# Kernel tuning notes

Measured on AMD Instinct MI355X. Metric: run time of the kernel, lower is better.

The kernel has to match this reference:

```python
import jax, jax.numpy as jnp
import numpy as np

NUM_HEADS = 8
HEAD_DIM = 64
AVG_K_LENGTH = 20
SCALE = 1.0 / (HEAD_DIM ** 0.5 * float(np.log(AVG_K_LENGTH)))  # 1/(sqrt(dim)*log(avg_k_length))


def setup_inputs() -> dict:
    key = jax.random.key(0)
    k1, k2, k3, k4 = jax.random.split(key, 4)
    B, HD, LQ, LK = 4, NUM_HEADS * HEAD_DIM, 2048, 2048
    q = jax.random.normal(k1, (B, HD, LQ), dtype=jnp.float32)
    k = jax.random.normal(k2, (B, HD, LK), dtype=jnp.float32)
    v = jax.random.normal(k3, (B, HD, LK), dtype=jnp.float32)
    k_length = jax.random.randint(k4, (B,), 512, LK + 1, dtype=jnp.int32)
    return {"q": q, "k": k, "v": v, "k_length": k_length}


def reference(q, k, v, k_length):
    b, hd, lq = q.shape
    lk = k.shape[-1]
    d = hd // NUM_HEADS
    # b (h d) l -> b h d l
    qh = q.reshape(b, NUM_HEADS, d, lq)
    kh = k.reshape(b, NUM_HEADS, d, lk)
    vh = v.reshape(b, NUM_HEADS, d, lk)
    # per-batch entropy-invariance scale: scale * log(k_length)
    s = SCALE * jnp.log(k_length.astype(jnp.float32))[:, None, None, None]  # (b,1,1,1)
    attn = jnp.einsum('bhdq,bhdk->bhqk', qh, kh)  # (b,h,lq,lk)
    attn = jax.nn.softmax(s * attn, axis=-1)
    out = jnp.einsum('bhqk,bhdk->bhdq', attn, vh)  # (b,h,d,lq)
    return out.reshape(b, hd, lq)
```

## Files before the change

### kernel.cpp

```cpp
#include <hip/hip_runtime.h>
#include <hip/hip_bf16.h>
#include <math.h>


typedef __attribute__((ext_vector_type(8))) short short8_t;
typedef __attribute__((ext_vector_type(4))) short short4_t;
typedef __attribute__((ext_vector_type(4))) float float4_t;

#define SEQ   2048
#define NBH   32
#define TQ    64
#define TK    64
#define NKT   (SEQ / TK)

__device__ __forceinline__ unsigned f2bf2u(float a, float b) {
#if __has_builtin(__builtin_amdgcn_cvt_pk_bf16_f32)
  typedef __bf16 bf16x2_t __attribute__((ext_vector_type(2)));
  union { bf16x2_t v; unsigned u; } cv;
  cv.v = __builtin_amdgcn_cvt_pk_bf16_f32(a, b);
  return cv.u;
#else
  union { float f; unsigned u; } x, y;
  x.f = a; y.f = b;
  unsigned ra = x.u + 0x7fffu + ((x.u >> 16) & 1u);
  unsigned rb = y.u + 0x7fffu + ((y.u >> 16) & 1u);
  return (ra >> 16) | (rb & 0xffff0000u);
#endif
}

__device__ __forceinline__ short f2bf1(float a) {
  return (short)(f2bf2u(a, a) & 0xffffu);
}

__device__ __forceinline__ float fast_exp2(float x) {
#if __has_builtin(__builtin_amdgcn_exp2f)
  return __builtin_amdgcn_exp2f(x);
#else
  return exp2f(x);
#endif
}

__device__ __forceinline__ void gld16(const void* g, void* l) {
  __builtin_amdgcn_global_load_lds(
      (const __attribute__((address_space(1))) void*)g,
      (__attribute__((address_space(3))) void*)l, 16, 0, 0);
}

__device__ __forceinline__ float4_t mfma16(short4_t a, short4_t b, float4_t c) {
#if __has_builtin(__builtin_amdgcn_mfma_f32_16x16x16bf16_1k)
  return __builtin_amdgcn_mfma_f32_16x16x16bf16_1k(a, b, c, 0, 0, 0);
#else
  asm("v_mfma_f32_16x16x16_bf16 %0, %1, %2, %0" : "+v"(c) : "v"(a), "v"(b));
  return c;
#endif
}

#define TSTR 68
__global__ __launch_bounds__(256, 8)
void eia_tcast_kernel(const float* __restrict__ in, unsigned short* __restrict__ out,
                      const int* __restrict__ klen, const int do_scale) {
  __shared__ __align__(16) short T[64 * TSTR];
  const int bh = blockIdx.x;
  const int b  = bh >> 3;
  const int l0 = blockIdx.y * 64;
  const int t  = threadIdx.x;
  const int lq = t & 63;
  const int dg = t >> 6;
  float c = 1.0f;
  if (do_scale)
    c = (1.4426950408889634f / (8.0f * 2.9957322735539909f)) * logf((float)klen[b]);
  const size_t ibase = ((size_t)bh * 64) * SEQ + (size_t)(l0 + lq);
#pragma unroll
  for (int dd = 0; dd < 16; dd += 4) {
    const int d = dg * 16 + dd;
    const float f0 = c * in[ibase + (size_t)(d + 0) * SEQ];
    const float f1 = c * in[ibase + (size_t)(d + 1) * SEQ];
    const float f2 = c * in[ibase + (size_t)(d + 2) * SEQ];
    const float f3 = c * in[ibase + (size_t)(d + 3) * SEQ];
    union { short4_t s; unsigned u[2]; } p;
    p.u[0] = f2bf2u(f0, f1);
    p.u[1] = f2bf2u(f2, f3);
    *(short4_t*)&T[lq * TSTR + d] = p.s;
  }
  __syncthreads();
#pragma unroll
  for (int rep = 0; rep < 2; ++rep) {
    const int id = rep * 256 + t;
    const int lr = id >> 3, ch = id & 7;
    union { short8_t v; short4_t h[2]; } o;
    o.h[0] = *(const short4_t*)&T[lr * TSTR + ch * 8];
    o.h[1] = *(const short4_t*)&T[lr * TSTR + ch * 8 + 4];
    *(short8_t*)&out[((size_t)bh * SEQ + l0 + lr) * 64 + ch * 8] = o.v;
  }
}

__global__ __launch_bounds__(256, 8)
void eia_vcast_kernel(const float* __restrict__ in, unsigned short* __restrict__ out) {
  const int i = blockIdx.x * 256 + threadIdx.x;
#pragma unroll
  for (int rep = 0; rep < 2; ++rep) {
    const size_t j = (size_t)(i + rep * 524288) * 4;
    const float4_t f = *(const float4_t*)&in[j];
    union { short4_t s; unsigned u[2]; } p;
    p.u[0] = f2bf2u(f[0], f[1]);
    p.u[1] = f2bf2u(f[2], f[3]);
    *(short4_t*)&out[j] = p.s;
  }
}

__global__ __launch_bounds__(256, 4)
void eia_attn_kernel(const unsigned short* __restrict__ Qt,
                     const unsigned short* __restrict__ Kt,
                     const unsigned short* __restrict__ Vb,
                     float* __restrict__ outg) {
  __shared__ __align__(16) short Ks[2 * TK * 64];
  __shared__ __align__(16) short Vs[2 * 64 * 64];

  const int tid  = threadIdx.x;
  const int bh   = blockIdx.x & 31;
  const int qt   = blockIdx.x >> 5;
  const int q0   = qt * TQ;
  const int w    = tid >> 6;
  const int lane = tid & 63;
  const int quad = lane >> 4;
  const int l16  = lane & 15;
  const int e3   = l16 & 7;
  const int qh   = quad >> 1;
  const int ql   = quad & 1;

  const int lr0 = w * 16 + (lane >> 3);
  const int lr1 = lr0 + 8;
  const int ch0 = (lane & 7) ^ (lr0 & 7);
  const char* kgp0 = (const char*)Kt + (size_t)bh * SEQ * 128 + (size_t)lr0 * 128 + ch0 * 16;
  const char* kgp1 = kgp0 + 8 * 128;
  const char* vgp0 = (const char*)Vb + (size_t)bh * 64 * (SEQ * 2) + (size_t)lr0 * (SEQ * 2) + ch0 * 16;
  const char* vgp1 = vgp0 + 8 * (SEQ * 2);
  short* const kdst0 = &Ks[(w * 16) * 64];
  short* const kdst1 = &Ks[(w * 16 + 8) * 64];
  short* const vdst0 = &Vs[(w * 16) * 64];
  short* const vdst1 = &Vs[(w * 16 + 8) * 64];

  const unsigned short* qrow = Qt + ((size_t)bh * SEQ + q0 + w * 16 + l16) * 64;
  short8_t qfrag[2];
#pragma unroll
  for (int s = 0; s < 2; ++s)
    qfrag[s] = *(const short8_t*)&qrow[s * 32 + quad * 8];

  int kaddr[4][2];
#pragma unroll
  for (int t = 0; t < 4; ++t)
#pragma unroll
    for (int s = 0; s < 2; ++s)
      kaddr[t][s] = (t * 16 + l16) * 64 + ((s * 4 + quad) ^ e3) * 8;
  int vcoff[4];
#pragma unroll
  for (int t = 0; t < 4; ++t)
    vcoff[t] = ((2 * t + qh) ^ e3) * 8 + ql * 4;

  float4_t oacc[4];
#pragma unroll
  for (int t = 0; t < 4; ++t) { oacc[t][0] = 0.f; oacc[t][1] = 0.f; oacc[t][2] = 0.f; oacc[t][3] = 0.f; }
  float lsum = 0.f;

  gld16(kgp0, kdst0); gld16(kgp1, kdst1);
  gld16(vgp0, vdst0); gld16(vgp1, vdst1);
  kgp0 += TK * 128; kgp1 += TK * 128; vgp0 += TK * 2; vgp1 += TK * 2;

  for (int kt = 0; kt < NKT; ++kt) {
    __syncthreads();

    if (kt < NKT - 1) {
      const int nb = ((kt + 1) & 1) * 4096;
      gld16(kgp0, kdst0 + nb); gld16(kgp1, kdst1 + nb);
      gld16(vgp0, vdst0 + nb); gld16(vgp1, vdst1 + nb);
      kgp0 += TK * 128; kgp1 += TK * 128; vgp0 += TK * 2; vgp1 += TK * 2;
    }
    const int cb = (kt & 1) * 4096;

    float4_t sacc[4];
#pragma unroll
    for (int t = 0; t < 4; ++t) { sacc[t][0] = 0.f; sacc[t][1] = 0.f; sacc[t][2] = 0.f; sacc[t][3] = 0.f; }
#pragma unroll
    for (int s = 0; s < 2; ++s)
#pragma unroll
      for (int t = 0; t < 4; ++t) {
        const short8_t kf = *(const short8_t*)&Ks[cb + kaddr[t][s]];
        sacc[t] = __builtin_amdgcn_mfma_f32_16x16x32_bf16(kf, qfrag[s], sacc[t], 0, 0, 0);
      }

    short4_t pb[4];
#pragma unroll
    for (int t = 0; t < 4; ++t) {
      const float e0 = fast_exp2(sacc[t][0]);
      const float e1 = fast_exp2(sacc[t][1]);
      const float e2 = fast_exp2(sacc[t][2]);
      const float e3f = fast_exp2(sacc[t][3]);
      lsum += (e0 + e1) + (e2 + e3f);
      union { short4_t s; unsigned u[2]; } p;
      p.u[0] = f2bf2u(e0, e1);
      p.u[1] = f2bf2u(e2, e3f);
      pb[t] = p.s;
    }

#pragma unroll
    for (int tt = 0; tt < 4; ++tt) {
      const short* vrow = &Vs[cb + (tt * 16 + l16) * 64];
#pragma unroll
      for (int t = 0; t < 4; ++t) {
        const short4_t vf = *(const short4_t*)&vrow[vcoff[t]];
        oacc[tt] = mfma16(vf, pb[t], oacc[tt]);
      }
    }
  }

  float lt = lsum;
  lt += __shfl_xor(lt, 16);
  lt += __shfl_xor(lt, 32);
  const float inv = 1.0f / lt;
  const size_t obase = (size_t)bh * 64 * SEQ + (size_t)(q0 + w * 16 + l16);
#pragma unroll
  for (int tt = 0; tt < 4; ++tt)
#pragma unroll
    for (int r = 0; r < 4; ++r)
      outg[obase + (size_t)(tt * 16 + quad * 4 + r) * SEQ] = oacc[tt][r] * inv;
}

#define DPAD  72
#define PPAD  68
__global__ __launch_bounds__(256, 5)
void eia_attn_fb(const float* __restrict__ qg, const float* __restrict__ kg,
                 const float* __restrict__ vg, const int* __restrict__ klen,
                 float* __restrict__ outg) {
  __shared__ __align__(16) short QPs[TQ * DPAD];
  __shared__ __align__(16) short Ksf[TK * DPAD];
  __shared__ __align__(16) short Vsf[64 * DPAD];

  const int tid  = threadIdx.x;
  const int bh   = blockIdx.x & 31;
  const int qt   = blockIdx.x >> 5;
  const int q0   = qt * TQ;
  const int w    = tid >> 6;
  const int lane = tid & 63;
  const int quad = lane >> 4;
  const int l16  = lane & 15;

  const size_t base = (size_t)bh * 64 * SEQ;
  const float c = (1.4426950408889634f / (8.0f * 2.9957322735539909f)) *
                  logf((float)klen[bh >> 3]);

#pragma unroll
  for (int it = 0; it < 2; ++it) {
    const int e = it * 4 + w;
    float f[8];
#pragma unroll
    for (int j = 0; j < 8; ++j)
      f[j] = c * qg[base + (size_t)(e * 8 + j) * SEQ + (size_t)(q0 + lane)];
    union { short8_t s8; unsigned u[4]; } t;
#pragma unroll
    for (int j = 0; j < 4; ++j) t.u[j] = f2bf2u(f[2 * j], f[2 * j + 1]);
    *(short8_t*)&QPs[lane * DPAD + e * 8] = t.s8;
  }
  __syncthreads();

  short8_t qfrag[2];
#pragma unroll
  for (int s = 0; s < 2; ++s)
    qfrag[s] = *(const short8_t*)&QPs[(w * 16 + l16) * DPAD + s * 32 + quad * 8];

  float4_t oacc[4];
#pragma unroll
  for (int t = 0; t < 4; ++t) { oacc[t][0] = 0.f; oacc[t][1] = 0.f; oacc[t][2] = 0.f; oacc[t][3] = 0.f; }
  float lsumv[4] = {0.f, 0.f, 0.f, 0.f};
  const int pbase = w * (16 * DPAD);

  for (int kt = 0; kt < NKT; ++kt) {
    const int k0 = kt * TK;
#pragma unroll
    for (int it = 0; it < 2; ++it) {
      float f[8];
#pragma unroll
      for (int j = 0; j < 8; ++j)
        f[j] = kg[base + (size_t)((it * 4 + w) * 8 + j) * SEQ + (size_t)(k0 + lane)];
      union { short8_t s8; unsigned u[4]; } t;
#pragma unroll
      for (int j = 0; j < 4; ++j) t.u[j] = f2bf2u(f[2 * j], f[2 * j + 1]);
      *(short8_t*)&Ksf[lane * DPAD + (it * 4 + w) * 8] = t.s8;
    }
#pragma unroll
    for (int it = 0; it < 4; ++it) {
      const int d = it * 16 + (w << 2) + (lane >> 4);
      const float4_t vv = *(const float4_t*)&vg[base + (size_t)d * SEQ + (size_t)(k0 + ((lane & 15) << 2))];
      union { short4_t s4; unsigned u[2]; } t;
      t.u[0] = f2bf2u(vv[0], vv[1]);
      t.u[1] = f2bf2u(vv[2], vv[3]);
      *(short4_t*)&Vsf[d * DPAD + ((lane & 15) << 2)] = t.s4;
    }
    __syncthreads();

    float4_t sacc[4];
#pragma unroll
    for (int t = 0; t < 4; ++t) { sacc[t][0] = 0.f; sacc[t][1] = 0.f; sacc[t][2] = 0.f; sacc[t][3] = 0.f; }
#pragma unroll
    for (int t = 0; t < 4; ++t)
#pragma unroll
      for (int s = 0; s < 2; ++s) {
        const short8_t bf = *(const short8_t*)&Ksf[(t * 16 + l16) * DPAD + s * 32 + quad * 8];
        sacc[t] = __builtin_amdgcn_mfma_f32_16x16x32_bf16(qfrag[s], bf, sacc[t], 0, 0, 0);
      }

#pragma unroll
    for (int r = 0; r < 4; ++r) {
      const float p0 = fast_exp2(sacc[0][r]);
      const float p1 = fast_exp2(sacc[1][r]);
      const float p2 = fast_exp2(sacc[2][r]);
      const float p3 = fast_exp2(sacc[3][r]);
      lsumv[r] += (p0 + p1) + (p2 + p3);
      const int prow = pbase + (quad * 4 + r) * PPAD + l16;
      QPs[prow +  0] = f2bf1(p0);
      QPs[prow + 16] = f2bf1(p1);
      QPs[prow + 32] = f2bf1(p2);
      QPs[prow + 48] = f2bf1(p3);
    }

#pragma unroll
    for (int s = 0; s < 2; ++s) {
      const short* pr = &QPs[pbase + l16 * PPAD + s * 32 + quad * 8];
      const short4_t plo = *(const short4_t*)pr;
      const short4_t phi = *(const short4_t*)(pr + 4);
      const short8_t pf = {plo[0], plo[1], plo[2], plo[3], phi[0], phi[1], phi[2], phi[3]};
#pragma unroll
      for (int t = 0; t < 4; ++t) {
        const short8_t vf = *(const short8_t*)&Vsf[(t * 16 + l16) * DPAD + s * 32 + quad * 8];
        oacc[t] = __builtin_amdgcn_mfma_f32_16x16x32_bf16(pf, vf, oacc[t], 0, 0, 0);
      }
    }
    __syncthreads();
  }

  float inv[4];
#pragma unroll
  for (int r = 0; r < 4; ++r) {
    float v = lsumv[r];
    v += __shfl_xor(v, 1);
    v += __shfl_xor(v, 2);
    v += __shfl_xor(v, 4);
    v += __shfl_xor(v, 8);
    inv[r] = 1.0f / v;
  }
#pragma unroll
  for (int t = 0; t < 4; ++t)
#pragma unroll
    for (int r = 0; r < 4; ++r)
      outg[base + (size_t)(t * 16 + l16) * SEQ +
           (size_t)(q0 + w * 16 + quad * 4 + r)] = oacc[t][r] * inv[r];
}

extern "C" void kernel_launch(void* const* d_in, const int* in_sizes, int n_in,
                              void* d_out, int out_size, void* d_ws, size_t ws_size,
                              hipStream_t stream) {
  const float* q  = (const float*)d_in[0];
  const float* k  = (const float*)d_in[1];
  const float* v  = (const float*)d_in[2];
  const int*   kl = (const int*)d_in[3];
  float* out = (float*)d_out;

  const size_t TEN = (size_t)NBH * SEQ * 64;
  const size_t need = 3 * TEN * sizeof(unsigned short);

  if (ws_size >= need) {
    unsigned short* Qt = (unsigned short*)d_ws;
    unsigned short* Kt = Qt + TEN;
    unsigned short* Vb = Kt + TEN;
    eia_tcast_kernel<<<dim3(32, 32), 256, 0, stream>>>(q, Qt, kl, 1);
    eia_tcast_kernel<<<dim3(32, 32), 256, 0, stream>>>(k, Kt, kl, 0);
    eia_vcast_kernel<<<2048, 256, 0, stream>>>(v, Vb);
    eia_attn_kernel<<<1024, 256, 0, stream>>>(Qt, Kt, Vb, out);
  } else {
    eia_attn_fb<<<1024, 256, 0, stream>>>(q, k, v, kl, out);
  }
}
```

Before: 151.3 us.

## Fuse Q cast into attention, merge K/V prep, double Q tile per block

Merges the K and V bf16 conversion into one prep kernel that writes pre-tiled, fragment-ordered layouts. The Q scale-and-cast now happens inside the attention kernel, which removes the Qt workspace and one launch. The Q tile per block grows to 128 rows, so each wave handles two 16-row groups and reuses every loaded K/V fragment twice. The row sums are now computed with an MFMA against a ones vector instead of VALU adds. In exchange, occupancy drops (launch bounds 2, 512 blocks) and register pressure rises.

```diff
diff --git a/kernel.cpp b/kernel.cpp
--- a/kernel.cpp
+++ b/kernel.cpp
@@ -9,7 +9,7 @@
 
 #define SEQ   2048
 #define NBH   32
-#define TQ    64
+#define TQ    128
 #define TK    64
 #define NKT   (SEQ / TK)
 
@@ -46,6 +46,10 @@
       (__attribute__((address_space(3))) void*)l, 16, 0, 0);
 }
 
+__device__ __forceinline__ float4_t mfma32(short8_t a, short8_t b, float4_t c) {
+  return __builtin_amdgcn_mfma_f32_16x16x32_bf16(a, b, c, 0, 0, 0);
+}
+
 __device__ __forceinline__ float4_t mfma16(short4_t a, short4_t b, float4_t c) {
 #if __has_builtin(__builtin_amdgcn_mfma_f32_16x16x16bf16_1k)
   return __builtin_amdgcn_mfma_f32_16x16x16bf16_1k(a, b, c, 0, 0, 0);
@@ -55,66 +59,76 @@
 #endif
 }
 
-#define TSTR 68
+#define PST 68
 __global__ __launch_bounds__(256, 8)
-void eia_tcast_kernel(const float* __restrict__ in, unsigned short* __restrict__ out,
-                      const int* __restrict__ klen, const int do_scale) {
-  __shared__ __align__(16) short T[64 * TSTR];
-  const int bh = blockIdx.x;
-  const int b  = bh >> 3;
-  const int l0 = blockIdx.y * 64;
-  const int t  = threadIdx.x;
-  const int lq = t & 63;
-  const int dg = t >> 6;
-  float c = 1.0f;
-  if (do_scale)
-    c = (1.4426950408889634f / (8.0f * 2.9957322735539909f)) * logf((float)klen[b]);
-  const size_t ibase = ((size_t)bh * 64) * SEQ + (size_t)(l0 + lq);
-#pragma unroll
-  for (int dd = 0; dd < 16; dd += 4) {
-    const int d = dg * 16 + dd;
-    const float f0 = c * in[ibase + (size_t)(d + 0) * SEQ];
-    const float f1 = c * in[ibase + (size_t)(d + 1) * SEQ];
-    const float f2 = c * in[ibase + (size_t)(d + 2) * SEQ];
-    const float f3 = c * in[ibase + (size_t)(d + 3) * SEQ];
-    union { short4_t s; unsigned u[2]; } p;
-    p.u[0] = f2bf2u(f0, f1);
-    p.u[1] = f2bf2u(f2, f3);
-    *(short4_t*)&T[lq * TSTR + d] = p.s;
-  }
-  __syncthreads();
-#pragma unroll
-  for (int rep = 0; rep < 2; ++rep) {
-    const int id = rep * 256 + t;
-    const int lr = id >> 3, ch = id & 7;
-    union { short8_t v; short4_t h[2]; } o;
-    o.h[0] = *(const short4_t*)&T[lr * TSTR + ch * 8];
-    o.h[1] = *(const short4_t*)&T[lr * TSTR + ch * 8 + 4];
-    *(short8_t*)&out[((size_t)bh * SEQ + l0 + lr) * 64 + ch * 8] = o.v;
-  }
-}
-
-__global__ __launch_bounds__(256, 8)
-void eia_vcast_kernel(const float* __restrict__ in, unsigned short* __restrict__ out) {
-  const int i = blockIdx.x * 256 + threadIdx.x;
-#pragma unroll
-  for (int rep = 0; rep < 2; ++rep) {
-    const size_t j = (size_t)(i + rep * 524288) * 4;
-    const float4_t f = *(const float4_t*)&in[j];
-    union { short4_t s; unsigned u[2]; } p;
-    p.u[0] = f2bf2u(f[0], f[1]);
-    p.u[1] = f2bf2u(f[2], f[3]);
-    *(short4_t*)&out[j] = p.s;
-  }
-}
-
-__global__ __launch_bounds__(256, 4)
-void eia_attn_kernel(const unsigned short* __restrict__ Qt,
-                     const unsigned short* __restrict__ Kt,
-                     const unsigned short* __restrict__ Vb,
+void eia_prep_kernel(const float* __restrict__ kg, const float* __restrict__ vg,
+                     unsigned short* __restrict__ Kt2, unsigned short* __restrict__ Vt2) {
+  __shared__ __align__(16) short T[64 * PST];
+  const int id  = blockIdx.x;
+  const int isV = id >> 10;
+  const int sub = id & 1023;
+  const int bh  = sub >> 5;
+  const int kt  = sub & 31;
+  const int t   = threadIdx.x;
+
+  if (!isV) {
+    const size_t ib = ((size_t)bh * 64) * SEQ + (size_t)(kt * 64) + (t & 63);
+    const int dg = t >> 6;
+#pragma unroll
+    for (int dd = 0; dd < 16; dd += 4) {
+      const int d = dg * 16 + dd;
+      const float f0 = kg[ib + (size_t)(d + 0) * SEQ];
+      const float f1 = kg[ib + (size_t)(d + 1) * SEQ];
+      const float f2 = kg[ib + (size_t)(d + 2) * SEQ];
+      const float f3 = kg[ib + (size_t)(d + 3) * SEQ];
+      union { short4_t s; unsigned u[2]; } p;
+      p.u[0] = f2bf2u(f0, f1);
+      p.u[1] = f2bf2u(f2, f3);
+      *(short4_t*)&T[(t & 63) * PST + d] = p.s;
+    }
+    __syncthreads();
+    unsigned short* outt = Kt2 + (size_t)(bh * 32 + kt) * 4096;
+#pragma unroll
+    for (int rep = 0; rep < 2; ++rep) {
+      const int id2 = rep * 256 + t;
+      const int lr = id2 & 63, ch = id2 >> 6;
+      union { short8_t v; short4_t h[2]; } o;
+      o.h[0] = *(const short4_t*)&T[lr * PST + ch * 8];
+      o.h[1] = *(const short4_t*)&T[lr * PST + ch * 8 + 4];
+      *(short8_t*)&outt[ch * 512 + lr * 8] = o.v;
+    }
+  } else {
+#pragma unroll
+    for (int rep = 0; rep < 4; ++rep) {
+      const int id2 = rep * 256 + t;
+      const int d = id2 >> 4, l4 = (id2 & 15) * 4;
+      const float4_t f = *(const float4_t*)&vg[((size_t)bh * 64 + d) * SEQ + kt * 64 + l4];
+      union { short4_t s; unsigned u[2]; } p;
+      p.u[0] = f2bf2u(f[0], f[1]);
+      p.u[1] = f2bf2u(f[2], f[3]);
+      *(short4_t*)&T[d * PST + l4] = p.s;
+    }
+    __syncthreads();
+    unsigned short* outt = Vt2 + (size_t)(bh * 32 + kt) * 4096;
+#pragma unroll
+    for (int rep = 0; rep < 2; ++rep) {
+      const int c = rep * 256 + t;
+      const int k4 = c >> 5, dp = c & 31;
+      union { short8_t v; short4_t h[2]; } o;
+      o.h[0] = *(const short4_t*)&T[(2 * dp) * PST + k4 * 4];
+      o.h[1] = *(const short4_t*)&T[(2 * dp + 1) * PST + k4 * 4];
+      *(short8_t*)&outt[k4 * 256 + dp * 8] = o.v;
+    }
+  }
+}
+
+__global__ __launch_bounds__(256, 2)
+void eia_attn_kernel(const float* __restrict__ qg,
+                     const unsigned short* __restrict__ Kt2,
+                     const unsigned short* __restrict__ Vt2,
+                     const int* __restrict__ klen,
                      float* __restrict__ outg) {
-  __shared__ __align__(16) short Ks[2 * TK * 64];
-  __shared__ __align__(16) short Vs[2 * 64 * 64];
+  __shared__ __align__(16) short SM[16384];
 
   const int tid  = threadIdx.x;
   const int bh   = blockIdx.x & 31;
@@ -124,105 +138,134 @@
   const int lane = tid & 63;
   const int quad = lane >> 4;
   const int l16  = lane & 15;
-  const int e3   = l16 & 7;
-  const int qh   = quad >> 1;
-  const int ql   = quad & 1;
-
-  const int lr0 = w * 16 + (lane >> 3);
-  const int lr1 = lr0 + 8;
-  const int ch0 = (lane & 7) ^ (lr0 & 7);
-  const char* kgp0 = (const char*)Kt + (size_t)bh * SEQ * 128 + (size_t)lr0 * 128 + ch0 * 16;
-  const char* kgp1 = kgp0 + 8 * 128;
-  const char* vgp0 = (const char*)Vb + (size_t)bh * 64 * (SEQ * 2) + (size_t)lr0 * (SEQ * 2) + ch0 * 16;
-  const char* vgp1 = vgp0 + 8 * (SEQ * 2);
-  short* const kdst0 = &Ks[(w * 16) * 64];
-  short* const kdst1 = &Ks[(w * 16 + 8) * 64];
-  short* const vdst0 = &Vs[(w * 16) * 64];
-  short* const vdst1 = &Vs[(w * 16 + 8) * 64];
-
-  const unsigned short* qrow = Qt + ((size_t)bh * SEQ + q0 + w * 16 + l16) * 64;
-  short8_t qfrag[2];
-#pragma unroll
-  for (int s = 0; s < 2; ++s)
-    qfrag[s] = *(const short8_t*)&qrow[s * 32 + quad * 8];
-
-  int kaddr[4][2];
-#pragma unroll
-  for (int t = 0; t < 4; ++t)
-#pragma unroll
-    for (int s = 0; s < 2; ++s)
-      kaddr[t][s] = (t * 16 + l16) * 64 + ((s * 4 + quad) ^ e3) * 8;
-  int vcoff[4];
-#pragma unroll
-  for (int t = 0; t < 4; ++t)
-    vcoff[t] = ((2 * t + qh) ^ e3) * 8 + ql * 4;
-
-  float4_t oacc[4];
-#pragma unroll
-  for (int t = 0; t < 4; ++t) { oacc[t][0] = 0.f; oacc[t][1] = 0.f; oacc[t][2] = 0.f; oacc[t][3] = 0.f; }
-  float lsum = 0.f;
-
-  gld16(kgp0, kdst0); gld16(kgp1, kdst1);
-  gld16(vgp0, vdst0); gld16(vgp1, vdst1);
-  kgp0 += TK * 128; kgp1 += TK * 128; vgp0 += TK * 2; vgp1 += TK * 2;
-
+
+  const float c = (1.4426950408889634f / (8.0f * 2.9957322735539909f)) *
+                  logf((float)klen[bh >> 3]);
+  const size_t qb = (size_t)bh * 64 * SEQ;
+
+#pragma unroll
+  for (int rep = 0; rep < 8; ++rep) {
+    const int id = rep * 256 + tid;
+    const int d  = id >> 5;
+    const int q4 = (id & 31) * 4;
+    const float4_t f = *(const float4_t*)&qg[qb + (size_t)d * SEQ + (size_t)(q0 + q4)];
+    SM[(q4 + 0) * 68 + d] = f2bf1(c * f[0]);
+    SM[(q4 + 1) * 68 + d] = f2bf1(c * f[1]);
+    SM[(q4 + 2) * 68 + d] = f2bf1(c * f[2]);
+    SM[(q4 + 3) * 68 + d] = f2bf1(c * f[3]);
+  }
+  __syncthreads();
+
+  short8_t qfrag[2][2];
+#pragma unroll
+  for (int g = 0; g < 2; ++g)
+#pragma unroll
+    for (int s = 0; s < 2; ++s) {
+      const short* qp = &SM[(w * 32 + g * 16 + l16) * 68 + s * 32 + quad * 8];
+      const short4_t lo = *(const short4_t*)qp;
+      const short4_t hi = *(const short4_t*)(qp + 4);
+      qfrag[g][s] = short8_t{lo[0], lo[1], lo[2], lo[3], hi[0], hi[1], hi[2], hi[3]};
+    }
+  __syncthreads();
+
+  const char* ktile = (const char*)Kt2 + (size_t)bh * 32 * 8192;
+  const char* vtile = (const char*)Vt2 + (size_t)bh * 32 * 8192;
+  const int i0 = 2 * w, i1 = 2 * w + 1;
+  const char* ks0 = ktile + i0 * 1024 + lane * 16;
+  const char* ks1 = ktile + i1 * 1024 + lane * 16;
+  const char* vs0 = vtile + i0 * 1024 + lane * 16;
+  const char* vs1 = vtile + i1 * 1024 + lane * 16;
+  short* const kd0 = &SM[i0 * 512];
+  short* const kd1 = &SM[i1 * 512];
+  short* const vd0 = &SM[8192 + i0 * 512];
+  short* const vd1 = &SM[8192 + i1 * 512];
+
+  const short* const kf0 = &SM[(0 * 4 + quad) * 512 + l16 * 8];
+  const short* const kf1 = &SM[(1 * 4 + quad) * 512 + l16 * 8];
+  const short* vfp[4];
+#pragma unroll
+  for (int t = 0; t < 4; ++t) vfp[t] = &SM[8192 + (t * 4 + quad) * 256 + l16 * 4];
+
+  const float4_t z4 = {0.f, 0.f, 0.f, 0.f};
+  float4_t oacc[2][4];
+#pragma unroll
+  for (int g = 0; g < 2; ++g)
+#pragma unroll
+    for (int t = 0; t < 4; ++t) oacc[g][t] = z4;
+  float4_t lacc[2] = {z4, z4};
+  const short one_bf = (short)0x3F80;
+  const short4_t ones4 = (l16 == 0) ? short4_t{one_bf, one_bf, one_bf, one_bf}
+                                    : short4_t{0, 0, 0, 0};
+
+  gld16(ks0, kd0); gld16(ks1, kd1);
+  gld16(vs0, vd0); gld16(vs1, vd1);
+  size_t goff = 8192;
+
+#pragma unroll 2
   for (int kt = 0; kt < NKT; ++kt) {
     __syncthreads();
 
     if (kt < NKT - 1) {
-      const int nb = ((kt + 1) & 1) * 4096;
-      gld16(kgp0, kdst0 + nb); gld16(kgp1, kdst1 + nb);
-      gld16(vgp0, vdst0 + nb); gld16(vgp1, vdst1 + nb);
-      kgp0 += TK * 128; kgp1 += TK * 128; vgp0 += TK * 2; vgp1 += TK * 2;
-    }
-    const int cb = (kt & 1) * 4096;
-
-    float4_t sacc[4];
-#pragma unroll
-    for (int t = 0; t < 4; ++t) { sacc[t][0] = 0.f; sacc[t][1] = 0.f; sacc[t][2] = 0.f; sacc[t][3] = 0.f; }
-#pragma unroll
-    for (int s = 0; s < 2; ++s)
+      const int pn = ((kt + 1) & 1) * 4096;
+      gld16(ks0 + goff, kd0 + pn); gld16(ks1 + goff, kd1 + pn);
+      gld16(vs0 + goff, vd0 + pn); gld16(vs1 + goff, vd1 + pn);
+      goff += 8192;
+    }
+    const int par = (kt & 1) * 4096;
+
+    float4_t sac[2][4];
+#pragma unroll
+    for (int t = 0; t < 4; ++t) {
+      const short8_t kv = *(const short8_t*)(kf0 + par + t * 128);
+      sac[0][t] = mfma32(kv, qfrag[0][0], z4);
+      sac[1][t] = mfma32(kv, qfrag[1][0], z4);
+    }
+#pragma unroll
+    for (int t = 0; t < 4; ++t) {
+      const short8_t kv = *(const short8_t*)(kf1 + par + t * 128);
+      sac[0][t] = mfma32(kv, qfrag[0][1], sac[0][t]);
+      sac[1][t] = mfma32(kv, qfrag[1][1], sac[1][t]);
+    }
+
+    short4_t pbf[2][4];
+#pragma unroll
+    for (int g = 0; g < 2; ++g)
 #pragma unroll
       for (int t = 0; t < 4; ++t) {
-        const short8_t kf = *(const short8_t*)&Ks[cb + kaddr[t][s]];
-        sacc[t] = __builtin_amdgcn_mfma_f32_16x16x32_bf16(kf, qfrag[s], sacc[t], 0, 0, 0);
+        const float e0 = fast_exp2(sac[g][t][0]);
+        const float e1 = fast_exp2(sac[g][t][1]);
+        const float e2 = fast_exp2(sac[g][t][2]);
+        const float e3 = fast_exp2(sac[g][t][3]);
+        union { short4_t s; unsigned u[2]; } p;
+        p.u[0] = f2bf2u(e0, e1);
+        p.u[1] = f2bf2u(e2, e3);
+        pbf[g][t] = p.s;
+        lacc[g] = mfma16(ones4, pbf[g][t], lacc[g]);
       }
 
-    short4_t pb[4];
 #pragma unroll
     for (int t = 0; t < 4; ++t) {
-      const float e0 = fast_exp2(sacc[t][0]);
-      const float e1 = fast_exp2(sacc[t][1]);
-      const float e2 = fast_exp2(sacc[t][2]);
-      const float e3f = fast_exp2(sacc[t][3]);
-      lsum += (e0 + e1) + (e2 + e3f);
-      union { short4_t s; unsigned u[2]; } p;
-      p.u[0] = f2bf2u(e0, e1);
-      p.u[1] = f2bf2u(e2, e3f);
-      pb[t] = p.s;
-    }
-
-#pragma unroll
-    for (int tt = 0; tt < 4; ++tt) {
-      const short* vrow = &Vs[cb + (tt * 16 + l16) * 64];
-#pragma unroll
-      for (int t = 0; t < 4; ++t) {
-        const short4_t vf = *(const short4_t*)&vrow[vcoff[t]];
-        oacc[tt] = mfma16(vf, pb[t], oacc[tt]);
+      const short* vfb = vfp[t] + par;
+#pragma unroll
+      for (int tt = 0; tt < 4; ++tt) {
+        const short4_t vv = *(const short4_t*)(vfb + tt * 64);
+        oacc[0][tt] = mfma16(vv, pbf[0][t], oacc[0][tt]);
+        oacc[1][tt] = mfma16(vv, pbf[1][t], oacc[1][tt]);
       }
     }
   }
 
-  float lt = lsum;
-  lt += __shfl_xor(lt, 16);
-  lt += __shfl_xor(lt, 32);
-  const float inv = 1.0f / lt;
-  const size_t obase = (size_t)bh * 64 * SEQ + (size_t)(q0 + w * 16 + l16);
-#pragma unroll
-  for (int tt = 0; tt < 4; ++tt)
-#pragma unroll
-    for (int r = 0; r < 4; ++r)
-      outg[obase + (size_t)(tt * 16 + quad * 4 + r) * SEQ] = oacc[tt][r] * inv;
+#pragma unroll
+  for (int g = 0; g < 2; ++g) {
+    const float ls  = __shfl(lacc[g][0], l16, 64);
+    const float inv = 1.0f / ls;
+    const size_t ob = qb + (size_t)(q0 + w * 32 + g * 16 + l16);
+#pragma unroll
+    for (int tt = 0; tt < 4; ++tt)
+#pragma unroll
+      for (int r = 0; r < 4; ++r)
+        outg[ob + (size_t)(tt * 16 + quad * 4 + r) * SEQ] = oacc[g][tt][r] * inv;
+  }
 }
 
 #define DPAD  72
@@ -231,14 +274,14 @@
 void eia_attn_fb(const float* __restrict__ qg, const float* __restrict__ kg,
                  const float* __restrict__ vg, const int* __restrict__ klen,
                  float* __restrict__ outg) {
-  __shared__ __align__(16) short QPs[TQ * DPAD];
-  __shared__ __align__(16) short Ksf[TK * DPAD];
+  __shared__ __align__(16) short QPs[64 * DPAD];
+  __shared__ __align__(16) short Ksf[64 * DPAD];
   __shared__ __align__(16) short Vsf[64 * DPAD];
 
   const int tid  = threadIdx.x;
   const int bh   = blockIdx.x & 31;
   const int qt   = blockIdx.x >> 5;
-  const int q0   = qt * TQ;
+  const int q0   = qt * 64;
   const int w    = tid >> 6;
   const int lane = tid & 63;
   const int quad = lane >> 4;
@@ -274,7 +317,7 @@
   const int pbase = w * (16 * DPAD);
 
   for (int kt = 0; kt < NKT; ++kt) {
-    const int k0 = kt * TK;
+    const int k0 = kt * 64;
 #pragma unroll
     for (int it = 0; it < 2; ++it) {
       float f[8];
@@ -305,7 +348,7 @@
 #pragma unroll
       for (int s = 0; s < 2; ++s) {
         const short8_t bf = *(const short8_t*)&Ksf[(t * 16 + l16) * DPAD + s * 32 + quad * 8];
-        sacc[t] = __builtin_amdgcn_mfma_f32_16x16x32_bf16(qfrag[s], bf, sacc[t], 0, 0, 0);
+        sacc[t] = mfma32(qfrag[s], bf, sacc[t]);
       }
 
 #pragma unroll
@@ -331,7 +374,7 @@
 #pragma unroll
       for (int t = 0; t < 4; ++t) {
         const short8_t vf = *(const short8_t*)&Vsf[(t * 16 + l16) * DPAD + s * 32 + quad * 8];
-        oacc[t] = __builtin_amdgcn_mfma_f32_16x16x32_bf16(pf, vf, oacc[t], 0, 0, 0);
+        oacc[t] = mfma32(pf, vf, oacc[t]);
       }
     }
     __syncthreads();
@@ -364,17 +407,14 @@
   const int*   kl = (const int*)d_in[3];
   float* out = (float*)d_out;
 
-  const size_t TEN = (size_t)NBH * SEQ * 64;
-  const size_t need = 3 * TEN * sizeof(unsigned short);
+  const size_t TEN  = (size_t)NBH * SEQ * 64;
+  const size_t need = 2 * TEN * sizeof(unsigned short);
 
   if (ws_size >= need) {
-    unsigned short* Qt = (unsigned short*)d_ws;
-    unsigned short* Kt = Qt + TEN;
-    unsigned short* Vb = Kt + TEN;
-    eia_tcast_kernel<<<dim3(32, 32), 256, 0, stream>>>(q, Qt, kl, 1);
-    eia_tcast_kernel<<<dim3(32, 32), 256, 0, stream>>>(k, Kt, kl, 0);
-    eia_vcast_kernel<<<2048, 256, 0, stream>>>(v, Vb);
-    eia_attn_kernel<<<1024, 256, 0, stream>>>(Qt, Kt, Vb, out);
+    unsigned short* Kt2 = (unsigned short*)d_ws;
+    unsigned short* Vt2 = Kt2 + TEN;
+    eia_prep_kernel<<<2048, 256, 0, stream>>>(k, v, Kt2, Vt2);
+    eia_attn_kernel<<<512, 256, 0, stream>>>(q, Kt2, Vt2, kl, out);
   } else {
     eia_attn_fb<<<1024, 256, 0, stream>>>(q, k, v, kl, out);
   }
```

Measured after the change: 143.3 us. 5.2% less time.
